# Performance work log

Measured on AMD Instinct MI355X. Metric: run time of the kernel, lower is better.

Reference implementation:

```python
import jax, jax.numpy as jnp
import numpy as np
import math

B, S, DM, L = 4, 512, 768, 2
DI, DS, K = 2 * DM, 16, 4          # mamba_ssm defaults: expand=2, d_state=16, d_conv=4
DTR = math.ceil(DM / 16)           # dt_rank = 48
F = 1


def setup_inputs() -> dict:
    key = jax.random.key(0)
    ks = iter(jax.random.split(key, 16))
    g = lambda shape, s=0.02: jax.random.normal(next(ks), shape, jnp.float32) * s
    # sinusoidal positional encoding (precomputed buffer)
    pos = np.arange(S)[:, None].astype(np.float32)
    div = np.exp(np.arange(0, DM, 2).astype(np.float32) * (-math.log(10000.0) / DM))
    pe = np.zeros((S, DM), np.float32)
    pe[:, 0::2] = np.sin(pos * div)
    pe[:, 1::2] = np.cos(pos * div)
    # S4D-real style A init
    A_log = jnp.broadcast_to(jnp.log(jnp.arange(1, DS + 1, dtype=jnp.float32)), (L, DI, DS))
    return dict(
        x=jax.random.normal(next(ks), (B, S, F), jnp.float32),
        w_in=g((DM, F)), b_in=jnp.zeros((DM,), jnp.float32),
        pe=jnp.asarray(pe)[None],                       # (1, S, DM)
        ln1_w=jnp.ones((L, DM)), ln1_b=jnp.zeros((L, DM)),
        w_inproj=g((L, 2 * DI, DM)),
        conv_w=g((L, DI, K), 0.1), conv_b=jnp.zeros((L, DI)),
        w_xproj=g((L, DTR + 2 * DS, DI)),
        w_dt=g((L, DI, DTR)), b_dt=jnp.full((L, DI), -4.0, jnp.float32),
        A_log=A_log, D=jnp.ones((L, DI)),
        w_outproj=g((L, DM, DI)),
        ln2_w=jnp.ones((L, DM)), ln2_b=jnp.zeros((L, DM)),
        ff_w1=g((L, 2 * DM, DM)), ff_b1=jnp.zeros((L, 2 * DM)),
        ff_w2=g((L, DM, 2 * DM)), ff_b2=jnp.zeros((L, DM)),
        lnf_w=jnp.ones((DM,)), lnf_b=jnp.zeros((DM,)),
        w_head=g((1, DM)), b_head=jnp.zeros((1,), jnp.float32),
    )


def _ln(x, w, b):
    mu = x.mean(-1, keepdims=True)
    v = ((x - mu) ** 2).mean(-1, keepdims=True)
    return (x - mu) * jax.lax.rsqrt(v + 1e-5) * w + b


def _mamba(x, w_inproj, conv_w, conv_b, w_xproj, w_dt, b_dt, A_log, D_, w_outproj):
    # x: (B, S, DM)
    Bsz = x.shape[0]
    xz = jnp.einsum('bsd,ed->bse', x, w_inproj)         # (B, S, 2*DI)
    xm, z = jnp.split(xz, 2, axis=-1)
    # causal depthwise conv1d over time
    xc = jax.lax.conv_general_dilated(
        xm.transpose(0, 2, 1), conv_w[:, None, :], (1,), [(K - 1, 0)],
        feature_group_count=DI, dimension_numbers=('NCH', 'OIH', 'NCH'))
    xc = jax.nn.silu((xc + conv_b[:, None]).transpose(0, 2, 1))  # (B, S, DI)
    dbc = jnp.einsum('bsd,ed->bse', xc, w_xproj)        # (B, S, DTR+2*DS)
    dt, Bm, Cm = dbc[..., :DTR], dbc[..., DTR:DTR + DS], dbc[..., DTR + DS:]
    delta = jax.nn.softplus(jnp.einsum('bsr,dr->bsd', dt, w_dt) + b_dt)  # (B, S, DI)
    A = -jnp.exp(A_log)                                 # (DI, DS)

    def step(h, inp):
        d_t, B_t, C_t, u_t = inp                        # (B,DI),(B,DS),(B,DS),(B,DI)
        h = h * jnp.exp(d_t[:, :, None] * A) + (d_t * u_t)[:, :, None] * B_t[:, None, :]
        return h, jnp.einsum('bds,bs->bd', h, C_t)

    h0 = jnp.zeros((Bsz, DI, DS), x.dtype)
    _, ys = jax.lax.scan(step, h0, (delta.transpose(1, 0, 2), Bm.transpose(1, 0, 2),
                                    Cm.transpose(1, 0, 2), xc.transpose(1, 0, 2)))
    y = ys.transpose(1, 0, 2) + xc * D_
    y = y * jax.nn.silu(z)
    return jnp.einsum('bsd,ed->bse', y, w_outproj)


def reference(x, w_in, b_in, pe, ln1_w, ln1_b, w_inproj, conv_w, conv_b, w_xproj,
              w_dt, b_dt, A_log, D, w_outproj, ln2_w, ln2_b, ff_w1, ff_b1,
              ff_w2, ff_b2, lnf_w, lnf_b, w_head, b_head):
    h = jnp.einsum('bsf,df->bsd', x, w_in) + b_in
    h = h + pe[:, :h.shape[1]]
    for l in range(L):  # fixed small layer count
        h = h + _mamba(_ln(h, ln1_w[l], ln1_b[l]), w_inproj[l], conv_w[l], conv_b[l],
                       w_xproj[l], w_dt[l], b_dt[l], A_log[l], D[l], w_outproj[l])
        f = _ln(h, ln2_w[l], ln2_b[l])
        f = jax.nn.gelu(jnp.einsum('bsd,ed->bse', f, ff_w1[l]) + ff_b1[l], approximate=False)
        h = h + jnp.einsum('bse,de->bsd', f, ff_w2[l]) + ff_b2[l]
    h = _ln(h, lnf_w, lnf_b)
    h = h.mean(axis=1)                                  # mean pool over time
    return jnp.einsum('bd,od->bo', h, w_head) + b_head
```

## Files before the change

kernel.cpp:

```cpp
#include <hip/hip_runtime.h>
#include <hip/hip_bf16.h>
#include <math.h>

#define B_ 4
#define S_ 512
#define DM_ 768
#define L_ 2
#define DI_ 1536
#define DS_ 16
#define KC_ 4
#define DTR_ 48
#define NSEG 32
#define TS 16
#define PMN_IP ((size_t)2048 * 2 * DI_)

typedef __hip_bfloat16 bf16;
typedef __attribute__((ext_vector_type(8))) short short8;
typedef __attribute__((ext_vector_type(4))) float f32x4;

#define GLDS16(g, l) __builtin_amdgcn_global_load_lds( \
    (const __attribute__((address_space(1))) void*)(g), \
    (__attribute__((address_space(3))) void*)(l), 16, 0, 0)

typedef struct { unsigned short x, y, z, w; } us4;
__device__ __forceinline__ void cast4(const float* __restrict__ s, bf16* __restrict__ d) {
  float4 v = *(const float4*)s;
  us4 o;
  o.x = __bfloat16_as_ushort(__float2bfloat16(v.x));
  o.y = __bfloat16_as_ushort(__float2bfloat16(v.y));
  o.z = __bfloat16_as_ushort(__float2bfloat16(v.z));
  o.w = __bfloat16_as_ushort(__float2bfloat16(v.w));
  *(us4*)d = o;
}
__device__ __forceinline__ void store4z(bf16* __restrict__ d) {
  us4 o; o.x = o.y = o.z = o.w = 0;
  *(us4*)d = o;
}

__global__ __launch_bounds__(256)
void k_init(const float* __restrict__ x, const float* __restrict__ w_in,
            const float* __restrict__ b_in, const float* __restrict__ pe,
            const float* __restrict__ lw, const float* __restrict__ lb,
            float* __restrict__ h, bf16* __restrict__ xout,
            const float* __restrict__ w_inproj, const float* __restrict__ w_outproj,
            const float* __restrict__ ff_w1, const float* __restrict__ ff_w2,
            const float* __restrict__ w_xproj, const float* __restrict__ w_dt,
            const float* __restrict__ A_log,
            bf16* __restrict__ wip, bf16* __restrict__ wop,
            bf16* __restrict__ wf1, bf16* __restrict__ wf2,
            bf16* __restrict__ wxp, bf16* __restrict__ wdtp,
            float* __restrict__ At) {
  if (blockIdx.x < 2048) {
    __shared__ float red1[4], red2[4];
    __shared__ float s_mu, s_rstd;
    int row = blockIdx.x;
    int s = row % S_;
    float xv = x[row];
    float v[3];
    float s1 = 0.f, s2 = 0.f;
#pragma unroll
    for (int j = 0; j < 3; ++j) {
      int d = threadIdx.x + j * 256;
      float t = xv * w_in[d] + b_in[d] + pe[s * DM_ + d];
      v[j] = t;
      s1 += t; s2 += t * t;
    }
    for (int off = 32; off; off >>= 1) { s1 += __shfl_down(s1, off); s2 += __shfl_down(s2, off); }
    if ((threadIdx.x & 63) == 0) { red1[threadIdx.x >> 6] = s1; red2[threadIdx.x >> 6] = s2; }
    __syncthreads();
    if (threadIdx.x == 0) {
      float t1 = red1[0] + red1[1] + red1[2] + red1[3];
      float t2 = red2[0] + red2[1] + red2[2] + red2[3];
      float mu = t1 * (1.f / DM_);
      float var = t2 * (1.f / DM_) - mu * mu;
      s_mu = mu;
      s_rstd = rsqrtf(var + 1e-5f);
    }
    __syncthreads();
    float mu = s_mu, rstd = s_rstd;
#pragma unroll
    for (int j = 0; j < 3; ++j) {
      int d = threadIdx.x + j * 256;
      h[(size_t)row * DM_ + d] = v[j];
      xout[(size_t)row * DM_ + d] = __float2bfloat16((v[j] - mu) * rstd * lw[d] + lb[d]);
    }
    return;
  }
  const int N0 = L_ * 2 * DI_ * DM_;
  const int N1 = L_ * DM_ * DI_;
  const int N2 = L_ * 2 * DM_ * DM_;
  const int N3 = L_ * DM_ * 2 * DM_;
  const int N4 = L_ * 128 * DI_;
  const int N5 = L_ * DI_ * 64;
  const int N6 = L_ * 16 * DI_;
  const int T4 = (N0 + N1 + N2 + N3 + N4 + N5) >> 2;
  int tid = (blockIdx.x - 2048) * 256 + threadIdx.x;
  int stride = 1024 * 256;
  for (int v = tid; v < T4; v += stride) {
    int j = v << 2;
    if (j < N0) { cast4(w_inproj + j, wip + j); continue; }
    j -= N0;
    if (j < N1) { cast4(w_outproj + j, wop + j); continue; }
    j -= N1;
    if (j < N2) { cast4(ff_w1 + j, wf1 + j); continue; }
    j -= N2;
    if (j < N3) { cast4(ff_w2 + j, wf2 + j); continue; }
    j -= N3;
    if (j < N4) {
      int col = j % DI_;
      int row = (j / DI_) & 127;
      int l = j / (128 * DI_);
      if (row < 80) cast4(&w_xproj[((size_t)l * 80 + row) * DI_ + col], wxp + j);
      else store4z(wxp + j);
      continue;
    }
    j -= N4;
    {
      int col = j & 63;
      int r = (j >> 6) % DI_;
      int l = j / (DI_ * 64);
      if (col < 48) cast4(&w_dt[((size_t)l * DI_ + r) * 48 + col], wdtp + j);
      else store4z(wdtp + j);
    }
  }
  for (int j = tid; j < N6; j += stride) {
    int d = j % DI_;
    int n = (j / DI_) & 15;
    int l = j / (16 * DI_);
    At[j] = -__expf(A_log[((size_t)l * DI_ + d) * 16 + n]);
  }
}

__global__ __launch_bounds__(256)
void k_lnred(const bf16* __restrict__ pxp, int KS,
             const float* __restrict__ hin, const float* __restrict__ bias,
             const float* __restrict__ lw, const float* __restrict__ lb,
             float* __restrict__ hout, bf16* __restrict__ xout) {
  __shared__ float red1[4], red2[4];
  __shared__ float s_mu, s_rstd;
  int row = blockIdx.x;
  float v[3];
  float s1 = 0.f, s2 = 0.f;
#pragma unroll
  for (int j = 0; j < 3; ++j) {
    int n = threadIdx.x + j * 256;
    float s = hin[(size_t)row * DM_ + n];
    if (bias) s += bias[n];
    for (int ks = 0; ks < KS; ++ks)
      s += __bfloat162float(pxp[(size_t)ks * 2048 * DM_ + (size_t)row * DM_ + n]);
    v[j] = s;
    s1 += s; s2 += s * s;
  }
  for (int off = 32; off; off >>= 1) { s1 += __shfl_down(s1, off); s2 += __shfl_down(s2, off); }
  if ((threadIdx.x & 63) == 0) { red1[threadIdx.x >> 6] = s1; red2[threadIdx.x >> 6] = s2; }
  __syncthreads();
  if (threadIdx.x == 0) {
    float t1 = red1[0] + red1[1] + red1[2] + red1[3];
    float t2 = red2[0] + red2[1] + red2[2] + red2[3];
    float mu = t1 * (1.f / DM_);
    float var = t2 * (1.f / DM_) - mu * mu;
    s_mu = mu;
    s_rstd = rsqrtf(var + 1e-5f);
  }
  __syncthreads();
  float mu = s_mu, rstd = s_rstd;
#pragma unroll
  for (int j = 0; j < 3; ++j) {
    int n = threadIdx.x + j * 256;
    hout[(size_t)row * DM_ + n] = v[j];
    xout[(size_t)row * DM_ + n] = __float2bfloat16((v[j] - mu) * rstd * lw[n] + lb[n]);
  }
}

__global__ void k_gelred(const bf16* __restrict__ pxp, const float* __restrict__ bias,
                         bf16* __restrict__ out) {
  int idx = blockIdx.x * 256 + threadIdx.x;
  if (idx >= 2048 * 2 * DM_) return;
  int n = idx % (2 * DM_);
  float s = __bfloat162float(pxp[idx]) +
            __bfloat162float(pxp[(size_t)2048 * 2 * DM_ + idx]) + bias[n];
  s = 0.5f * s * (1.f + erff(s * 0.70710678118654752f));
  out[idx] = __float2bfloat16(s);
}

__global__ void k_conv_silu(const bf16* __restrict__ pip, const float* __restrict__ cw,
                            const float* __restrict__ cb, bf16* __restrict__ xcb) {
  int idx = blockIdx.x * 256 + threadIdx.x;
  if (idx >= B_ * S_ * (DI_ / 2)) return;
  int d2 = idx % (DI_ / 2);
  int d = d2 * 2;
  int t = idx / (DI_ / 2);
  int s = t % S_;
  int b = t / S_;
  float a0 = cb[d], a1 = cb[d + 1];
  const bf16* p0 = pip + (size_t)(b * S_) * (2 * DI_) + d;
  const bf16* p1 = p0 + PMN_IP;
#pragma unroll
  for (int k = 0; k < KC_; ++k) {
    int ss = s - (KC_ - 1) + k;
    if (ss >= 0) {
      ushort2 u0 = *(const ushort2*)&p0[(size_t)ss * (2 * DI_)];
      ushort2 u1 = *(const ushort2*)&p1[(size_t)ss * (2 * DI_)];
      float x0 = __bfloat162float(__ushort_as_bfloat16(u0.x)) +
                 __bfloat162float(__ushort_as_bfloat16(u1.x));
      float x1 = __bfloat162float(__ushort_as_bfloat16(u0.y)) +
                 __bfloat162float(__ushort_as_bfloat16(u1.y));
      a0 = fmaf(x0, cw[d * KC_ + k], a0);
      a1 = fmaf(x1, cw[(d + 1) * KC_ + k], a1);
    }
  }
  float v0 = a0 / (1.f + expf(-a0));
  float v1 = a1 / (1.f + expf(-a1));
  ushort2 o;
  o.x = __bfloat16_as_ushort(__float2bfloat16(v0));
  o.y = __bfloat16_as_ushort(__float2bfloat16(v1));
  *(ushort2*)&xcb[(size_t)t * DI_ + d] = o;
}

__global__ __launch_bounds__(256)
void k_scanA(const float* __restrict__ delta, const bf16* __restrict__ xcb,
             const float* __restrict__ bc, const float* __restrict__ At,
             const float* __restrict__ Dv,
             float* __restrict__ ylocal, float* __restrict__ cumd,
             float* __restrict__ hend) {
  int b = blockIdx.y;
  int seg = blockIdx.z;
  int d = blockIdx.x * 256 + threadIdx.x;
  int s0 = seg * TS;

  float A[16], hst[16];
#pragma unroll
  for (int n = 0; n < 16; ++n) {
    A[n] = At[(size_t)n * DI_ + d];
    hst[n] = 0.f;
  }
  float Dd = Dv[d];
  float cd = 0.f;

  const float* dp = delta + ((size_t)(b * S_ + s0)) * DI_ + d;
  const bf16* up = xcb + ((size_t)(b * S_ + s0)) * DI_ + d;
  const float* bp = bc + ((size_t)(b * S_ + s0)) * 32;
  float* yp = ylocal + ((size_t)(b * S_ + s0)) * DI_ + d;
  float* cp = cumd + ((size_t)(b * S_ + s0)) * DI_ + d;

  float dl_next = dp[0];
  float u_next = __bfloat162float(up[0]);
#pragma unroll 4
  for (int s = 0; s < TS; ++s) {
    float dl = dl_next, u = u_next;
    if (s + 1 < TS) {
      dl_next = dp[(size_t)(s + 1) * DI_];
      u_next = __bfloat162float(up[(size_t)(s + 1) * DI_]);
    }
    cd += dl;
    float dlu = dl * u;
    float y = 0.f;
#pragma unroll
    for (int n = 0; n < 16; ++n) {
      float e = __expf(dl * A[n]);
      hst[n] = fmaf(hst[n], e, dlu * bp[s * 32 + n]);
      y = fmaf(hst[n], bp[s * 32 + 16 + n], y);
    }
    yp[(size_t)s * DI_] = fmaf(u, Dd, y);
    cp[(size_t)s * DI_] = cd;
  }
  float* hp = hend + ((size_t)(b * NSEG + seg) * 16) * DI_ + d;
#pragma unroll
  for (int n = 0; n < 16; ++n) hp[(size_t)n * DI_] = hst[n];
}

__global__ void k_scanB(const float* __restrict__ hend, const float* __restrict__ cumd,
                        const float* __restrict__ At, float* __restrict__ h0seg) {
  int idx = blockIdx.x * 256 + threadIdx.x;
  if (idx >= B_ * 16 * DI_) return;
  int d = idx % DI_;
  int r = idx / DI_;
  int n = r & 15;
  int b = r >> 4;
  float A = At[(size_t)n * DI_ + d];
  float h0 = 0.f;
  for (int seg = 0; seg < NSEG; ++seg) {
    size_t o = ((size_t)(b * NSEG + seg) * 16 + n) * DI_ + d;
    h0seg[o] = h0;
    float cdt = cumd[((size_t)(b * S_ + seg * TS + TS - 1)) * DI_ + d];
    h0 = h0 * __expf(A * cdt) + hend[o];
  }
}

__global__ __launch_bounds__(256)
void k_scanC(const float* __restrict__ ylocal, const float* __restrict__ cumd,
             const float* __restrict__ bc, const float* __restrict__ At,
             const float* __restrict__ h0seg, const bf16* __restrict__ pip,
             bf16* __restrict__ yb16) {
  int d = blockIdx.x * 256 + threadIdx.x;
  int t = blockIdx.y;
  int b = blockIdx.z;
  int seg = t / TS;
  size_t o = ((size_t)(b * S_ + t)) * DI_ + d;
  float y = ylocal[o];
  if (seg) {
    float cd = cumd[o];
    const float* Cp = bc + ((size_t)(b * S_ + t)) * 32 + 16;
    const float* Hb = h0seg + ((size_t)(b * NSEG + seg) * 16) * DI_ + d;
#pragma unroll
    for (int n = 0; n < 16; ++n)
      y += Cp[n] * __expf(At[(size_t)n * DI_ + d] * cd) * Hb[(size_t)n * DI_];
  }
  size_t oz = ((size_t)(b * S_ + t)) * (2 * DI_) + DI_ + d;
  float z = __bfloat162float(pip[oz]) + __bfloat162float(pip[PMN_IP + oz]);
  float sig = 1.f / (1.f + __expf(-z));
  yb16[o] = __float2bfloat16(y * (z * sig));
}

__global__ void k_head1(const bf16* __restrict__ hf, const float* __restrict__ wh,
                        float* __restrict__ partial) {
  __shared__ float red[4];
  int b = blockIdx.y, j = blockIdx.x;
  const bf16* base = hf + ((size_t)b * S_ + j * 32) * DM_;
  float acc = 0.f;
  for (int i = threadIdx.x; i < 32 * DM_; i += 256) {
    int dd = i - (i / DM_) * DM_;
    acc += __bfloat162float(base[i]) * wh[dd];
  }
  for (int off = 32; off; off >>= 1) acc += __shfl_down(acc, off);
  if ((threadIdx.x & 63) == 0) red[threadIdx.x >> 6] = acc;
  __syncthreads();
  if (threadIdx.x == 0)
    partial[b * 16 + j] = red[0] + red[1] + red[2] + red[3];
}

__global__ void k_head2(const float* __restrict__ partial, const float* __restrict__ bh,
                        float* __restrict__ out) {
  int b = threadIdx.x;
  if (b < B_) {
    float acc = 0.f;
    for (int j = 0; j < 16; ++j) acc += partial[b * 16 + j];
    out[b] = acc * (1.f / S_) + bh[0];
  }
}

template <int EPI>
__global__ __launch_bounds__(256)
void k_gemm_mfma(const bf16* __restrict__ A, int lda,
                 const bf16* __restrict__ W, int ldw,
                 const float* __restrict__ bias,
                 void* __restrict__ out1,
                 int ldc, int N, int Kdim, int pmn) {
  __shared__ short As[2][8192];
  __shared__ short Bs[2][8192];

  int nwg = gridDim.x * gridDim.y;
  int orig = blockIdx.y * gridDim.x + blockIdx.x;
  int wg = (nwg % 8 == 0) ? ((orig & 7) * (nwg >> 3) + (orig >> 3)) : orig;
  int m0 = (wg / gridDim.x) * 128;
  int n0 = (wg % gridDim.x) * 128;

  int lane = threadIdx.x & 63;
  int wid = threadIdx.x >> 6;
  int wm = wid >> 1, wn = wid & 1;
  int lr = lane & 15;
  int ch = lane >> 4;
  int koff = blockIdx.z * Kdim;

  f32x4 acc[4][4];
#pragma unroll
  for (int i = 0; i < 4; ++i)
#pragma unroll
    for (int j = 0; j < 4; ++j) {
      acc[i][j][0] = 0.f; acc[i][j][1] = 0.f; acc[i][j][2] = 0.f; acc[i][j][3] = 0.f;
    }

#define GSTAGE(bb, kt)                                                            \
  {                                                                               \
    int k0 = koff + (kt) * 64;                                                    \
    _Pragma("unroll")                                                             \
    for (int c0 = 0; c0 < 4; ++c0) {                                              \
      int c = c0 * 256 + (int)threadIdx.x;                                        \
      int row = c & 127, chk = c >> 7;                                            \
      GLDS16(A + (size_t)(m0 + row) * lda + k0 + chk * 8,                         \
             (char*)&As[bb][0] + c * 16);                                         \
      GLDS16(W + (size_t)(n0 + row) * ldw + k0 + chk * 8,                         \
             (char*)&Bs[bb][0] + c * 16);                                         \
    }                                                                             \
  }

  int nt = Kdim / 64;
  GSTAGE(0, 0);

  for (int t = 0; t < nt; ++t) {
    int buf = t & 1;
    if (t + 1 < nt) {
      GSTAGE(buf ^ 1, t + 1);
      asm volatile("s_waitcnt vmcnt(8)" ::: "memory");
    } else {
      asm volatile("s_waitcnt vmcnt(0)" ::: "memory");
    }
    __builtin_amdgcn_s_barrier();
    __builtin_amdgcn_sched_barrier(0);

    short8 a0[4], a1[4], b0[4], b1[4];
#pragma unroll
    for (int f = 0; f < 4; ++f) {
      a0[f] = *(const short8*)&As[buf][(ch * 128 + wm * 64 + f * 16 + lr) * 8];
      b0[f] = *(const short8*)&Bs[buf][(ch * 128 + wn * 64 + f * 16 + lr) * 8];
    }
    __builtin_amdgcn_sched_barrier(0);
#pragma unroll
    for (int f = 0; f < 4; ++f) {
      a1[f] = *(const short8*)&As[buf][((4 + ch) * 128 + wm * 64 + f * 16 + lr) * 8];
      b1[f] = *(const short8*)&Bs[buf][((4 + ch) * 128 + wn * 64 + f * 16 + lr) * 8];
    }
    asm volatile("s_waitcnt lgkmcnt(8)" ::: "memory");
    __builtin_amdgcn_sched_barrier(0);
    __builtin_amdgcn_s_setprio(1);
#pragma unroll
    for (int i = 0; i < 4; ++i)
#pragma unroll
      for (int j = 0; j < 4; ++j)
        acc[i][j] = __builtin_amdgcn_mfma_f32_16x16x32_bf16(a0[i], b0[j], acc[i][j], 0, 0, 0);
    __builtin_amdgcn_sched_barrier(0);
    asm volatile("s_waitcnt lgkmcnt(0)" ::: "memory");
    __builtin_amdgcn_sched_barrier(0);
#pragma unroll
    for (int i = 0; i < 4; ++i)
#pragma unroll
      for (int j = 0; j < 4; ++j)
        acc[i][j] = __builtin_amdgcn_mfma_f32_16x16x32_bf16(a1[i], b1[j], acc[i][j], 0, 0, 0);
    __builtin_amdgcn_s_setprio(0);
    __builtin_amdgcn_sched_barrier(0);
    __builtin_amdgcn_s_barrier();
  }
#undef GSTAGE

#pragma unroll
  for (int i = 0; i < 4; ++i) {
#pragma unroll
    for (int j = 0; j < 4; ++j) {
      int nl = wn * 64 + j * 16 + (lane & 15);
      int n = n0 + nl;
#pragma unroll
      for (int q = 0; q < 4; ++q) {
        int m = m0 + wm * 64 + i * 16 + (lane >> 4) * 4 + q;
        float v = acc[i][j][q];
        if (EPI == 0) {
          ((float*)out1)[(size_t)m * ldc + n] = v;
        } else if (EPI == 3) {
          v += bias[n];
          v = (v > 20.f) ? v : log1pf(expf(v));
          ((float*)out1)[(size_t)m * ldc + n] = v;
        } else if (EPI == 5) {
          ((float*)out1)[(size_t)blockIdx.z * pmn + (size_t)m * N + n] = v;
        } else if (EPI == 6) {
          ((bf16*)out1)[(size_t)m * ldc + n] = __float2bfloat16(v);
        } else if (EPI == 7) {
          ((bf16*)out1)[(size_t)blockIdx.z * pmn + (size_t)m * N + n] = __float2bfloat16(v);
        }
      }
    }
  }
}

__global__ void k_xreduce(const float* __restrict__ pxp, bf16* __restrict__ dtp,
                          float* __restrict__ bcb) {
  int idx = blockIdx.x * 256 + threadIdx.x;
  if (idx >= 2048 * 128) return;
  int m = idx >> 7, n = idx & 127;
  float s = 0.f;
#pragma unroll
  for (int k = 0; k < 8; ++k) s += pxp[(size_t)k * 2048 * 128 + idx];
  if (n < 64) dtp[m * 64 + n] = __float2bfloat16(n < 48 ? s : 0.f);
  if (n >= 48 && n < 80) bcb[m * 32 + (n - 48)] = s;
}


extern "C" void kernel_launch(void* const* d_in, const int* in_sizes, int n_in,
                              void* d_out, int out_size, void* d_ws, size_t ws_size,
                              hipStream_t stream) {
  const float* x        = (const float*)d_in[0];
  const float* w_in     = (const float*)d_in[1];
  const float* b_in     = (const float*)d_in[2];
  const float* pe       = (const float*)d_in[3];
  const float* ln1_w    = (const float*)d_in[4];
  const float* ln1_b    = (const float*)d_in[5];
  const float* w_inproj = (const float*)d_in[6];
  const float* conv_w   = (const float*)d_in[7];
  const float* conv_b   = (const float*)d_in[8];
  const float* w_xproj  = (const float*)d_in[9];
  const float* w_dt     = (const float*)d_in[10];
  const float* b_dt     = (const float*)d_in[11];
  const float* A_log    = (const float*)d_in[12];
  const float* Dv       = (const float*)d_in[13];
  const float* w_outproj= (const float*)d_in[14];
  const float* ln2_w    = (const float*)d_in[15];
  const float* ln2_b    = (const float*)d_in[16];
  const float* ff_w1    = (const float*)d_in[17];
  const float* ff_b1    = (const float*)d_in[18];
  const float* ff_w2    = (const float*)d_in[19];
  const float* ff_b2    = (const float*)d_in[20];
  const float* lnf_w    = (const float*)d_in[21];
  const float* lnf_b    = (const float*)d_in[22];
  const float* w_head   = (const float*)d_in[23];
  const float* b_head   = (const float*)d_in[24];
  float* out = (float*)d_out;

  const int M = B_ * S_;

  float* wsf = (float*)d_ws;
  float* h    = wsf; wsf += (size_t)M * DM_;
  float* bc   = wsf; wsf += (size_t)M * 32;
  float* dlt  = wsf; wsf += (size_t)M * DI_;
  float* cumd = wsf; wsf += (size_t)M * DI_;
  float* hend = wsf; wsf += (size_t)B_ * NSEG * DI_ * 16;
  float* h0sg = wsf; wsf += (size_t)B_ * NSEG * DI_ * 16;
  float* pxp  = wsf; wsf += (size_t)4 * M * 2 * DM_;
  float* At   = wsf; wsf += (size_t)L_ * 16 * DI_;
  float* part = wsf; wsf += 64;
  bf16* wsb = (bf16*)wsf;
  bf16* xln16 = wsb; wsb += (size_t)M * DM_;
  bf16* pip   = wsb; wsb += 2 * PMN_IP;
  bf16* xcb   = wsb; wsb += (size_t)M * DI_;
  bf16* dtp   = wsb; wsb += (size_t)M * 64;
  bf16* yb16  = wsb; wsb += (size_t)M * DI_;
  bf16* ffh16 = wsb; wsb += (size_t)M * DI_;
  bf16* wip   = wsb; wsb += (size_t)L_ * 2 * DI_ * DM_;
  bf16* wxp   = wsb; wsb += (size_t)L_ * 128 * DI_;
  bf16* wdtp  = wsb; wsb += (size_t)L_ * DI_ * 64;
  bf16* wop   = wsb; wsb += (size_t)L_ * DM_ * DI_;
  bf16* wf1   = wsb; wsb += (size_t)L_ * 2 * DM_ * DM_;
  bf16* wf2   = wsb; wsb += (size_t)L_ * DM_ * 2 * DM_;

  float* ylocal = dlt;
  bf16* pxp16 = (bf16*)pxp;

  dim3 blk(256);

  k_init<<<2048 + 1024, blk, 0, stream>>>(
      x, w_in, b_in, pe, ln1_w, ln1_b, h, xln16,
      w_inproj, w_outproj, ff_w1, ff_w2, w_xproj, w_dt, A_log,
      wip, wop, wf1, wf2, wxp, wdtp, At);

  for (int l = 0; l < L_; ++l) {
    const float* Atl = At + (size_t)l * 16 * DI_;

    k_gemm_mfma<7><<<dim3(2 * DI_ / 128, M / 128, 2), blk, 0, stream>>>(
        xln16, DM_, wip + (size_t)l * 2 * DI_ * DM_, DM_, nullptr,
        pip, 2 * DI_, 2 * DI_, DM_ / 2, (int)PMN_IP);

    k_conv_silu<<<(B_ * S_ * (DI_ / 2) + 255) / 256, blk, 0, stream>>>(
        pip, conv_w + l * DI_ * KC_, conv_b + l * DI_, xcb);

    k_gemm_mfma<5><<<dim3(1, M / 128, 8), blk, 0, stream>>>(
        xcb, DI_, wxp + (size_t)l * 128 * DI_, DI_, nullptr,
        pxp, 128, 128, DI_ / 8, M * 128);
    k_xreduce<<<(M * 128) / 256, blk, 0, stream>>>(pxp, dtp, bc);

    k_gemm_mfma<3><<<dim3(DI_ / 128, M / 128), blk, 0, stream>>>(
        dtp, 64, wdtp + (size_t)l * DI_ * 64, 64, b_dt + l * DI_,
        dlt, DI_, DI_, 64, 0);

    k_scanA<<<dim3(DI_ / 256, B_, NSEG), blk, 0, stream>>>(
        dlt, xcb, bc, Atl, Dv + l * DI_, ylocal, cumd, hend);
    k_scanB<<<(B_ * 16 * DI_ + 255) / 256, blk, 0, stream>>>(hend, cumd, Atl, h0sg);
    k_scanC<<<dim3(DI_ / 256, S_, B_), blk, 0, stream>>>(
        ylocal, cumd, bc, Atl, h0sg, pip, yb16);

    k_gemm_mfma<7><<<dim3(DM_ / 128, M / 128, 4), blk, 0, stream>>>(
        yb16, DI_, wop + (size_t)l * DM_ * DI_, DI_, nullptr,
        pxp16, DM_, DM_, DI_ / 4, M * DM_);
    k_lnred<<<M, blk, 0, stream>>>(pxp16, 4, h, nullptr,
                                   ln2_w + l * DM_, ln2_b + l * DM_, h, xln16);

    k_gemm_mfma<7><<<dim3(2 * DM_ / 128, M / 128, 2), blk, 0, stream>>>(
        xln16, DM_, wf1 + (size_t)l * 2 * DM_ * DM_, DM_, nullptr,
        pxp16, 2 * DM_, 2 * DM_, DM_ / 2, M * 2 * DM_);
    k_gelred<<<(M * 2 * DM_) / 256, blk, 0, stream>>>(pxp16, ff_b1 + l * 2 * DM_, ffh16);

    k_gemm_mfma<7><<<dim3(DM_ / 128, M / 128, 4), blk, 0, stream>>>(
        ffh16, 2 * DM_, wf2 + (size_t)l * DM_ * 2 * DM_, 2 * DM_, nullptr,
        pxp16, DM_, DM_, DI_ / 4, M * DM_);
    const float* nlw = (l + 1 < L_) ? ln1_w + (l + 1) * DM_ : lnf_w;
    const float* nlb = (l + 1 < L_) ? ln1_b + (l + 1) * DM_ : lnf_b;
    k_lnred<<<M, blk, 0, stream>>>(pxp16, 4, h, ff_b2 + l * DM_, nlw, nlb, h, xln16);
  }

  k_head1<<<dim3(16, B_), blk, 0, stream>>>(xln16, w_head, part);
  k_head2<<<1, 64, 0, stream>>>(part, b_head, out);
}
```

Before: 497.7 us.

## Fuse dt projection and softplus into scan, fold head dot into final layernorm

```diff
diff --git a/kernel.cpp b/kernel.cpp
--- a/kernel.cpp
+++ b/kernel.cpp
@@ -49,7 +49,7 @@
             bf16* __restrict__ wip, bf16* __restrict__ wop,
             bf16* __restrict__ wf1, bf16* __restrict__ wf2,
             bf16* __restrict__ wxp, bf16* __restrict__ wdtp,
-            float* __restrict__ At) {
+            float* __restrict__ At, float* __restrict__ part) {
   if (blockIdx.x < 2048) {
     __shared__ float red1[4], red2[4];
     __shared__ float s_mu, s_rstd;
@@ -86,6 +86,7 @@
     }
     return;
   }
+  if (blockIdx.x == 2048 && threadIdx.x < B_) part[threadIdx.x] = 0.f;
   const int N0 = L_ * 2 * DI_ * DM_;
   const int N1 = L_ * DM_ * DI_;
   const int N2 = L_ * 2 * DM_ * DM_;
@@ -135,7 +136,8 @@
 void k_lnred(const bf16* __restrict__ pxp, int KS,
              const float* __restrict__ hin, const float* __restrict__ bias,
              const float* __restrict__ lw, const float* __restrict__ lb,
-             float* __restrict__ hout, bf16* __restrict__ xout) {
+             float* __restrict__ hout, bf16* __restrict__ xout,
+             const float* __restrict__ wh, float* __restrict__ headp) {
   __shared__ float red1[4], red2[4];
   __shared__ float s_mu, s_rstd;
   int row = blockIdx.x;
@@ -164,11 +166,22 @@
   }
   __syncthreads();
   float mu = s_mu, rstd = s_rstd;
+  float hacc = 0.f;
 #pragma unroll
   for (int j = 0; j < 3; ++j) {
     int n = threadIdx.x + j * 256;
+    float vl = (v[j] - mu) * rstd * lw[n] + lb[n];
     hout[(size_t)row * DM_ + n] = v[j];
-    xout[(size_t)row * DM_ + n] = __float2bfloat16((v[j] - mu) * rstd * lw[n] + lb[n]);
+    xout[(size_t)row * DM_ + n] = __float2bfloat16(vl);
+    if (headp) hacc += vl * wh[n];
+  }
+  if (headp) {
+    __syncthreads();
+    for (int off = 32; off; off >>= 1) hacc += __shfl_down(hacc, off);
+    if ((threadIdx.x & 63) == 0) red1[threadIdx.x >> 6] = hacc;
+    __syncthreads();
+    if (threadIdx.x == 0)
+      atomicAdd(headp + row / S_, red1[0] + red1[1] + red1[2] + red1[3]);
   }
 }
 
@@ -218,9 +231,10 @@
 }
 
 __global__ __launch_bounds__(256)
-void k_scanA(const float* __restrict__ delta, const bf16* __restrict__ xcb,
-             const float* __restrict__ bc, const float* __restrict__ At,
-             const float* __restrict__ Dv,
+void k_scanA(const bf16* __restrict__ dtp, const bf16* __restrict__ wdt_l,
+             const float* __restrict__ bdt_l,
+             const bf16* __restrict__ xcb, const float* __restrict__ bc,
+             const float* __restrict__ At, const float* __restrict__ Dv,
              float* __restrict__ ylocal, float* __restrict__ cumd,
              float* __restrict__ hend) {
   int b = blockIdx.y;
@@ -234,24 +248,35 @@
     A[n] = At[(size_t)n * DI_ + d];
     hst[n] = 0.f;
   }
+  float wdt[48];
+  {
+    const bf16* wrow = wdt_l + (size_t)d * 64;
+#pragma unroll
+    for (int k = 0; k < 48; ++k) wdt[k] = __bfloat162float(wrow[k]);
+  }
+  float bdt = bdt_l[d];
   float Dd = Dv[d];
   float cd = 0.f;
 
-  const float* dp = delta + ((size_t)(b * S_ + s0)) * DI_ + d;
+  const unsigned int* dru = (const unsigned int*)(dtp) + (size_t)(b * S_ + s0) * 32;
   const bf16* up = xcb + ((size_t)(b * S_ + s0)) * DI_ + d;
   const float* bp = bc + ((size_t)(b * S_ + s0)) * 32;
   float* yp = ylocal + ((size_t)(b * S_ + s0)) * DI_ + d;
   float* cp = cumd + ((size_t)(b * S_ + s0)) * DI_ + d;
 
-  float dl_next = dp[0];
   float u_next = __bfloat162float(up[0]);
 #pragma unroll 4
   for (int s = 0; s < TS; ++s) {
-    float dl = dl_next, u = u_next;
-    if (s + 1 < TS) {
-      dl_next = dp[(size_t)(s + 1) * DI_];
-      u_next = __bfloat162float(up[(size_t)(s + 1) * DI_]);
-    }
+    float u = u_next;
+    if (s + 1 < TS) u_next = __bfloat162float(up[(size_t)(s + 1) * DI_]);
+    float acc = bdt;
+#pragma unroll
+    for (int kk = 0; kk < 24; ++kk) {
+      unsigned int w2 = dru[s * 32 + kk];
+      acc = fmaf(__uint_as_float(w2 << 16), wdt[2 * kk], acc);
+      acc = fmaf(__uint_as_float(w2 & 0xffff0000u), wdt[2 * kk + 1], acc);
+    }
+    float dl = (acc > 20.f) ? acc : log1pf(__expf(acc));
     cd += dl;
     float dlu = dl * u;
     float y = 0.f;
@@ -312,31 +337,10 @@
   yb16[o] = __float2bfloat16(y * (z * sig));
 }
 
-__global__ void k_head1(const bf16* __restrict__ hf, const float* __restrict__ wh,
-                        float* __restrict__ partial) {
-  __shared__ float red[4];
-  int b = blockIdx.y, j = blockIdx.x;
-  const bf16* base = hf + ((size_t)b * S_ + j * 32) * DM_;
-  float acc = 0.f;
-  for (int i = threadIdx.x; i < 32 * DM_; i += 256) {
-    int dd = i - (i / DM_) * DM_;
-    acc += __bfloat162float(base[i]) * wh[dd];
-  }
-  for (int off = 32; off; off >>= 1) acc += __shfl_down(acc, off);
-  if ((threadIdx.x & 63) == 0) red[threadIdx.x >> 6] = acc;
-  __syncthreads();
-  if (threadIdx.x == 0)
-    partial[b * 16 + j] = red[0] + red[1] + red[2] + red[3];
-}
-
-__global__ void k_head2(const float* __restrict__ partial, const float* __restrict__ bh,
+__global__ void k_head2(const float* __restrict__ part, const float* __restrict__ bh,
                         float* __restrict__ out) {
   int b = threadIdx.x;
-  if (b < B_) {
-    float acc = 0.f;
-    for (int j = 0; j < 16; ++j) acc += partial[b * 16 + j];
-    out[b] = acc * (1.f / S_) + bh[0];
-  }
+  if (b < B_) out[b] = part[b] * (1.f / S_) + bh[0];
 }
 
 template <int EPI>
@@ -508,7 +512,7 @@
   float* wsf = (float*)d_ws;
   float* h    = wsf; wsf += (size_t)M * DM_;
   float* bc   = wsf; wsf += (size_t)M * 32;
-  float* dlt  = wsf; wsf += (size_t)M * DI_;
+  float* ylocal = wsf; wsf += (size_t)M * DI_;
   float* cumd = wsf; wsf += (size_t)M * DI_;
   float* hend = wsf; wsf += (size_t)B_ * NSEG * DI_ * 16;
   float* h0sg = wsf; wsf += (size_t)B_ * NSEG * DI_ * 16;
@@ -529,7 +533,6 @@
   bf16* wf1   = wsb; wsb += (size_t)L_ * 2 * DM_ * DM_;
   bf16* wf2   = wsb; wsb += (size_t)L_ * DM_ * 2 * DM_;
 
-  float* ylocal = dlt;
   bf16* pxp16 = (bf16*)pxp;
 
   dim3 blk(256);
@@ -537,7 +540,7 @@
   k_init<<<2048 + 1024, blk, 0, stream>>>(
       x, w_in, b_in, pe, ln1_w, ln1_b, h, xln16,
       w_inproj, w_outproj, ff_w1, ff_w2, w_xproj, w_dt, A_log,
-      wip, wop, wf1, wf2, wxp, wdtp, At);
+      wip, wop, wf1, wf2, wxp, wdtp, At, part);
 
   for (int l = 0; l < L_; ++l) {
     const float* Atl = At + (size_t)l * 16 * DI_;
@@ -554,12 +557,9 @@
         pxp, 128, 128, DI_ / 8, M * 128);
     k_xreduce<<<(M * 128) / 256, blk, 0, stream>>>(pxp, dtp, bc);
 
-    k_gemm_mfma<3><<<dim3(DI_ / 128, M / 128), blk, 0, stream>>>(
-        dtp, 64, wdtp + (size_t)l * DI_ * 64, 64, b_dt + l * DI_,
-        dlt, DI_, DI_, 64, 0);
-
     k_scanA<<<dim3(DI_ / 256, B_, NSEG), blk, 0, stream>>>(
-        dlt, xcb, bc, Atl, Dv + l * DI_, ylocal, cumd, hend);
+        dtp, wdtp + (size_t)l * DI_ * 64, b_dt + l * DI_,
+        xcb, bc, Atl, Dv + l * DI_, ylocal, cumd, hend);
     k_scanB<<<(B_ * 16 * DI_ + 255) / 256, blk, 0, stream>>>(hend, cumd, Atl, h0sg);
     k_scanC<<<dim3(DI_ / 256, S_, B_), blk, 0, stream>>>(
         ylocal, cumd, bc, Atl, h0sg, pip, yb16);
@@ -568,7 +568,8 @@
         yb16, DI_, wop + (size_t)l * DM_ * DI_, DI_, nullptr,
         pxp16, DM_, DM_, DI_ / 4, M * DM_);
     k_lnred<<<M, blk, 0, stream>>>(pxp16, 4, h, nullptr,
-                                   ln2_w + l * DM_, ln2_b + l * DM_, h, xln16);
+                                   ln2_w + l * DM_, ln2_b + l * DM_, h, xln16,
+                                   nullptr, nullptr);
 
     k_gemm_mfma<7><<<dim3(2 * DM_ / 128, M / 128, 2), blk, 0, stream>>>(
         xln16, DM_, wf1 + (size_t)l * 2 * DM_ * DM_, DM_, nullptr,
@@ -580,9 +581,11 @@
         pxp16, DM_, DM_, DI_ / 4, M * DM_);
     const float* nlw = (l + 1 < L_) ? ln1_w + (l + 1) * DM_ : lnf_w;
     const float* nlb = (l + 1 < L_) ? ln1_b + (l + 1) * DM_ : lnf_b;
-    k_lnred<<<M, blk, 0, stream>>>(pxp16, 4, h, ff_b2 + l * DM_, nlw, nlb, h, xln16);
-  }
-
-  k_head1<<<dim3(16, B_), blk, 0, stream>>>(xln16, w_head, part);
+    const float* whp = (l + 1 < L_) ? nullptr : w_head;
+    float* hpp = (l + 1 < L_) ? nullptr : part;
+    k_lnred<<<M, blk, 0, stream>>>(pxp16, 4, h, ff_b2 + l * DM_, nlw, nlb, h, xln16,
+                                   whp, hpp);
+  }
+
   k_head2<<<1, 64, 0, stream>>>(part, b_head, out);
 }
```

After: 489.2 us. About the same (-1.7%).
